# Kernel optimization log

Measured on AMD Instinct MI355X. Metric: run time of the kernel, lower is better.

## Reference

```python
import jax, jax.numpy as jnp
import numpy as np

V, E, H = 50000, 256, 256   # vocab, emb_dim, hid_dim
R, S, W = 64, 32, 64        # reviews, sentences/review, words/sentence
UF = 20                     # user feature dim


def _bigru_last(x, wih, whh, bih, bhh):
    """Bidirectional GRU over x [B,T,D]; returns sum of final hidden states of
    the two directions, shape [B,H]. Params stacked over direction axis 0."""
    Hh = whh.shape[-1]

    def onedir(xd, wi, wh, bi, bh):
        gx = jnp.einsum('btd,gd->btg', xd, wi) + bi  # [B,T,3H] input gates precomputed

        def step(h, gxt):
            gh = h @ wh.T + bh
            r = jax.nn.sigmoid(gxt[:, :Hh] + gh[:, :Hh])
            z = jax.nn.sigmoid(gxt[:, Hh:2 * Hh] + gh[:, Hh:2 * Hh])
            n = jnp.tanh(gxt[:, 2 * Hh:] + r * gh[:, 2 * Hh:])
            return (1.0 - z) * n + z * h, None

        h0 = jnp.zeros((xd.shape[0], Hh), xd.dtype)
        hT, _ = jax.lax.scan(step, h0, jnp.swapaxes(gx, 0, 1))
        return hT

    return (onedir(x, wih[0], whh[0], bih[0], bhh[0])
            + onedir(x[:, ::-1], wih[1], whh[1], bih[1], bhh[1]))


def setup_inputs() -> dict:
    key = jax.random.key(0)
    ks = iter(jax.random.split(key, 40))

    def wmat(shape, scale=0.05):
        return jax.random.normal(next(ks), shape, jnp.float32) * scale

    inp = {}
    inp['inputs'] = jax.random.randint(next(ks), (R, S, W), 0, V)
    inp['sent_lengths'] = jax.random.randint(next(ks), (R, S), 1, W)
    inp['sent_counts'] = jax.random.randint(next(ks), (R,), 1, S)
    inp['user_feats'] = jax.random.normal(next(ks), (R, UF), jnp.float32)
    inp['embed'] = wmat((V, E))
    for name, din in (('wg', E), ('sg', H), ('rg', H + UF)):
        inp[name + '_wih'] = wmat((2, 3 * H, din))
        inp[name + '_whh'] = wmat((2, 3 * H, H))
        inp[name + '_bih'] = jnp.zeros((2, 3 * H), jnp.float32)
        inp[name + '_bhh'] = jnp.zeros((2, 3 * H), jnp.float32)
    inp['rfc_w1'] = wmat((H // 2, H + UF)); inp['rfc_b1'] = jnp.zeros((H // 2,), jnp.float32)
    inp['rfc_w2'] = wmat((1, H // 2));      inp['rfc_b2'] = jnp.zeros((1,), jnp.float32)
    inp['pfc_w1'] = wmat((H // 2, H));      inp['pfc_b1'] = jnp.zeros((H // 2,), jnp.float32)
    inp['pfc_w2'] = wmat((9, H // 2));      inp['pfc_b2'] = jnp.zeros((9,), jnp.float32)
    inp['uf_w'] = jnp.ones((UF,), jnp.float32)  # user_feats_weights
    return inp


def reference(inputs, sent_lengths, sent_counts, user_feats, embed,
              wg_wih, wg_whh, wg_bih, wg_bhh,
              sg_wih, sg_whh, sg_bih, sg_bhh,
              rg_wih, rg_whh, rg_bih, rg_bhh,
              rfc_w1, rfc_b1, rfc_w2, rfc_b2,
              pfc_w1, pfc_b1, pfc_w2, pfc_b2, uf_w):
    Rr, Sr, Wr = inputs.shape
    emb = embed[inputs]  # [R,S,W,E]  (dropout = identity in eval mode)
    # word-level bi-GRU, all R*S sentences batched together
    sent = _bigru_last(emb.reshape(Rr * Sr, Wr, emb.shape[-1]),
                       wg_wih, wg_whh, wg_bih, wg_bhh).reshape(Rr, Sr, -1)
    # sentence-level bi-GRU, batch over reviews
    rev = _bigru_last(sent, sg_wih, sg_whh, sg_bih, sg_bhh)  # [R,H]
    # F.normalize(user_feats) * user_feats_weights
    nrm = jnp.maximum(jnp.linalg.norm(user_feats, axis=-1, keepdims=True), 1e-12)
    p_batch = jnp.concatenate([rev, (user_feats / nrm) * uf_w], axis=-1)  # [R,H+20]
    r_stars = (jax.nn.selu(p_batch @ rfc_w1.T + rfc_b1) @ rfc_w2.T + rfc_b2)[:, 0]  # [R]
    # review-level bi-GRU over the sequence of reviews (batch 1)
    doc = _bigru_last(p_batch[None], rg_wih, rg_whh, rg_bih, rg_bhh)[0]  # [H]
    p_stars = jax.nn.selu(doc @ pfc_w1.T + pfc_b1) @ pfc_w2.T + pfc_b2  # [9]
    return p_stars, r_stars
```

## Files before the change

kernel.cpp:

```cpp
#include <hip/hip_runtime.h>
#include <math.h>

#define R_ 64
#define S_ 32
#define W_ 64
#define H_ 256
#define UF_ 20
#define TC 4

typedef short bf16x8 __attribute__((ext_vector_type(8)));
typedef float f32x4  __attribute__((ext_vector_type(4)));

#define MFMA(a,b,c) __builtin_amdgcn_mfma_f32_16x16x32_bf16((a),(b),(c),0,0,0)

typedef const unsigned int __attribute__((address_space(1)))* gp_t;
typedef unsigned int __attribute__((address_space(3)))* lp_t;
#define GLOAD16(SRC, DST) \
  __builtin_amdgcn_global_load_lds((gp_t)(const void*)(SRC), (lp_t)(void*)(DST), 16, 0, 0)

#define SW(r) ((((r)>>1)&7)<<3)

#define BFRAG(ff) ((ff) < 40 ? Breg[(ff) < 40 ? (ff) : 0] \
                 : *(const bf16x8*)&Bl[w][(ff) >= 40 ? (ff)-40 : 0][l*8])

__device__ __forceinline__ float sigf(float x){ return 1.0f/(1.0f+__expf(-x)); }
__device__ __forceinline__ float tanhf_(float x){ float e=__expf(2.0f*x); return 1.0f-2.0f/(e+1.0f); }
__device__ __forceinline__ float seluf_(float x){
  const float sc=1.0507009873554805f, al=1.6732632423543772f;
  return x>0.0f ? sc*x : sc*al*(expf(x)-1.0f);
}
__device__ __forceinline__ short tobf(float f){
  unsigned u=__float_as_uint(f); u += 0x7fffu + ((u>>16)&1u); return (short)(u>>16);
}
__device__ __forceinline__ float bf2f(short s){
  return __uint_as_float(((unsigned)(unsigned short)s) << 16);
}
__device__ __forceinline__ unsigned pk2(float a, float b){
  return (unsigned)(unsigned short)tobf(a) | ((unsigned)(unsigned short)tobf(b) << 16);
}

__global__ void prep_word_w(const float* __restrict__ wih, const float* __restrict__ whh,
                            short* __restrict__ Bw)
{
  int idx = blockIdx.x*256 + threadIdx.x;
  int lane = idx & 63;
  int rest = idx >> 6;
  int f  = rest % 6;  rest /= 6;
  int kt = rest % 16; rest /= 16;
  int w  = rest % 8;
  int d  = rest / 8;
  int gate = f >> 1;
  int j = 32*w + (f&1)*16 + (lane&15);
  int row = gate*256 + j;
  const float* W = (kt < 8 ? wih : whh) + (size_t)d*768*256;
  int k = (kt&7)*32 + (lane>>4)*8;
  short* dst = Bw + ((((size_t)(d*8 + w)*16 + kt)*6 + f)*64 + lane)*8;
#pragma unroll
  for (int jj=0;jj<8;jj++) dst[jj] = tobf(W[(size_t)row*256 + k + jj]);
}

__global__ void prep_rnn_w(const float* __restrict__ whh, short* __restrict__ Bs)
{
  int idx = blockIdx.x*256 + threadIdx.x;
  int lane = idx & 63;
  int rest = idx >> 6;
  int f  = rest % 6; rest /= 6;
  int kt = rest % 8; rest /= 8;
  int w  = rest % 8;
  int d  = rest / 8;
  int j = 32*w + (f&1)*16 + (lane&15);
  int row = (f>>1)*256 + j;
  const float* W = whh + (size_t)d*768*256;
  int k = kt*32 + (lane>>4)*8;
  short* dst = Bs + ((((size_t)(d*8 + w)*8 + kt)*6 + f)*64 + lane)*8;
#pragma unroll
  for (int jj=0;jj<8;jj++) dst[jj] = tobf(W[(size_t)row*256 + k + jj]);
}

__global__ void prep_gemm_w(const float* __restrict__ Wsrc, short* __restrict__ Bg)
{
  int idx = blockIdx.x*256 + threadIdx.x;
  int lane = idx & 63;
  int rest = idx >> 6;
  int kt = rest % 8;
  int nt = rest / 8;
  int n = nt*16 + (lane&15);
  int k = kt*32 + (lane>>4)*8;
  short* dst = Bg + (((size_t)nt*8 + kt)*64 + lane)*8;
#pragma unroll
  for (int jj=0;jj<8;jj++) dst[jj] = tobf(Wsrc[(size_t)n*256 + k + jj]);
}

__global__ void prep_embb(const float* __restrict__ E, short* __restrict__ O, int M)
{
  const int t = blockIdx.x*256 + threadIdx.x;
  const int row = t >> 5, c0 = (t & 31)*8;
  const int r = row < M ? row : M - 1;
  const float* s = E + (size_t)r*256 + c0;
  float4 v0 = *(const float4*)(s);
  float4 v1 = *(const float4*)(s + 4);
  uint4 u;
  u.x = pk2(v0.x, v0.y); u.y = pk2(v0.z, v0.w);
  u.z = pk2(v1.x, v1.y); u.w = pk2(v1.z, v1.w);
  *(uint4*)&O[(size_t)row*256 + c0] = u;
}

__global__ __launch_bounds__(256) void gemm_gxu(
    const short* __restrict__ Ab, const float* __restrict__ Af,
    const int* __restrict__ toks, const short* __restrict__ Bg,
    const float* __restrict__ bih, const float* __restrict__ bhh,
    short* __restrict__ C, long Czoff,
    int mode, int t0, int Mclamp, int Cstride)
{
  const int z  = blockIdx.z;
  const int m0 = blockIdx.x * 64;
  const int yt = blockIdx.y * 8;
  const int ntb = (mode == 2 ? z*48 : 0) + yt;
  const int tid = threadIdx.x;
  const int w = tid >> 6, l = tid & 63;
  const int c = l & 15, q = l >> 4;
  __shared__ short As[64][264];
  {
    const int row = tid >> 2, c0 = (tid & 3) * 64;
    if (mode == 0) {
      const uint4* s = (const uint4*)(Ab + (size_t)(m0+row)*256 + c0);
#pragma unroll
      for (int i = 0; i < 8; i++) *(uint4*)&As[row][c0 + i*8] = s[i];
    } else {
      int r;
      if (mode == 1) {
        r = m0 + row; if (r >= Mclamp) r = Mclamp - 1;
      } else {
        const int rr = m0 + row;
        const int s_ = rr / TC, i_ = rr % TC;
        const int wd = z ? (63 - (t0 + i_)) : (t0 + i_);
        r = toks[s_*64 + wd];
      }
      const float* s = Af + (size_t)r*256 + c0;
#pragma unroll
      for (int i = 0; i < 8; i++) {
        float4 v0 = *(const float4*)(s + i*8);
        float4 v1 = *(const float4*)(s + i*8 + 4);
        uint4 u;
        u.x = pk2(v0.x, v0.y); u.y = pk2(v0.z, v0.w);
        u.z = pk2(v1.x, v1.y); u.w = pk2(v1.z, v1.w);
        *(uint4*)&As[row][c0 + i*8] = u;
      }
    }
  }
  float bias[2];
#pragma unroll
  for (int nt = 0; nt < 2; nt++) {
    const int coln = (yt + 2*w + nt)*16 + c;
    const int bidx = (mode == 2 ? z*768 : 0) + coln;
    bias[nt] = bih[bidx] + ((bidx % 768) < 512 ? bhh[bidx] : 0.0f);
  }
  __syncthreads();
  f32x4 acc[4][2];
#pragma unroll
  for (int a = 0; a < 4; a++) { acc[a][0] = (f32x4)0.f; acc[a][1] = (f32x4)0.f; }
#pragma unroll
  for (int kt = 0; kt < 8; kt++) {
    const int ko = kt*32 + q*8;
    bf16x8 a0 = *(const bf16x8*)&As[ 0+c][ko];
    bf16x8 a1 = *(const bf16x8*)&As[16+c][ko];
    bf16x8 a2 = *(const bf16x8*)&As[32+c][ko];
    bf16x8 a3 = *(const bf16x8*)&As[48+c][ko];
    bf16x8 b0 = *(const bf16x8*)&Bg[(((size_t)(ntb + 2*w    )*8 + kt)*64 + l)*8];
    bf16x8 b1 = *(const bf16x8*)&Bg[(((size_t)(ntb + 2*w + 1)*8 + kt)*64 + l)*8];
    acc[0][0]=MFMA(a0,b0,acc[0][0]); acc[1][0]=MFMA(a1,b0,acc[1][0]);
    acc[2][0]=MFMA(a2,b0,acc[2][0]); acc[3][0]=MFMA(a3,b0,acc[3][0]);
    acc[0][1]=MFMA(a0,b1,acc[0][1]); acc[1][1]=MFMA(a1,b1,acc[1][1]);
    acc[2][1]=MFMA(a2,b1,acc[2][1]); acc[3][1]=MFMA(a3,b1,acc[3][1]);
  }
  short* Cz = C + (size_t)z * Czoff;
#pragma unroll
  for (int mt = 0; mt < 4; mt++)
#pragma unroll
  for (int nt = 0; nt < 2; nt++)
#pragma unroll
  for (int rg = 0; rg < 4; rg++)
    Cz[(size_t)(m0 + mt*16 + q*4 + rg)*Cstride + (yt + 2*w + nt)*16 + c] =
        tobf(acc[mt][nt][rg] + bias[nt]);
}

__device__ __forceinline__ void stage_issue(
    short* dstbase,
    int mode, int d, int g, int w, int l,
    int nwords, int t0, int tt,
    const int* tokp, const short* gxF, const short* gxB)
{
  const char* bF = (const char*)gxF;
  const char* bB = (const char*)gxB;
#pragma unroll
  for (int i = 0; i < 3; i++) {
    const int off = i*1024 + l*16;
    const int rl  = (off >= 1536) ? 1 : 0;
    const int col = off - rl*1536;
    const char* src;
    if (mode == 0) {
      const int tx  = d ? (nwords - 1 - tt) : tt;
      const int tok = tokp[(2*w + rl)*64 + tx];
      src = bF + (size_t)tok*3072 + d*1536 + col;
    } else if (mode == 1) {
      const int ri = (g*16 + 2*w + rl)*TC + (tt - t0);
      src = (d ? bB : bF) + (size_t)ri*1536 + col;
    } else {
      const int se  = d ? (nwords - 1 - tt) : tt;
      const int row = g*16 + 2*w + rl;
      src = bF + ((size_t)row*nwords + se)*3072 + (size_t)d*1536 + col;
    }
    GLOAD16(src, dstbase + (size_t)w*1536 + i*512);
  }
}

__global__ __launch_bounds__(512, 2) void gru_rec(
    const int* __restrict__ toks,
    const short* __restrict__ gxF, const short* __restrict__ gxB,
    const short* __restrict__ Bh, int wstride, int koff,
    const float* __restrict__ bhh,
    float* __restrict__ hstate, int NS,
    int t0, int nsteps, int mode, int nwords)
{
  const int d = blockIdx.x & 1;
  const int g = blockIdx.x >> 1;
  const int tid = threadIdx.x;
  const int w = tid >> 6, l = tid & 63;
  const int c = l & 15, q = l >> 4;

  __shared__ short gbuf[2][16][768];
  __shared__ short hbf[2][16][264];
  __shared__ short Bl[8][8][512];
  __shared__ int   tokL[1024];

  if (mode == 0)
    for (int i = tid; i < 1024; i += 512) tokL[i] = toks[(size_t)g*1024 + i];

  bf16x8 Breg[40];
  {
    const short* Bb = Bh + (size_t)(d*8 + w)*wstride + (size_t)koff*3072 + l*8;
#pragma unroll
    for (int ff = 0; ff < 48; ff++) {
      bf16x8 v = *(const bf16x8*)(Bb + ff*512);
      if (ff < 40) Breg[ff] = v;
      else *(bf16x8*)&Bl[w][ff-40][l*8] = v;
    }
  }

  float bNH[2];
#pragma unroll
  for (int jt = 0; jt < 2; jt++)
    bNH[jt] = bhh[d*768 + 512 + 32*w + jt*16 + c];

  float hst[2][4];
  const int cur0 = t0 & 1;
  if (t0 == 0) {
#pragma unroll
    for (int a = 0; a < 2; a++)
#pragma unroll
    for (int r = 0; r < 4; r++) hst[a][r] = 0.0f;
  } else {
#pragma unroll
    for (int jt = 0; jt < 2; jt++)
#pragma unroll
    for (int rg = 0; rg < 4; rg++)
      hst[jt][rg] = hstate[((size_t)d*NS + g*16 + q*4 + rg)*256 + 32*w + jt*16 + c];
  }
#pragma unroll
  for (int jt = 0; jt < 2; jt++)
#pragma unroll
  for (int rg = 0; rg < 4; rg++)
    hbf[cur0][q*4 + rg][32*w + jt*16 + c] = tobf(hst[jt][rg]);

  stage_issue((short*)gbuf[cur0], mode, d, g, w, l, nwords, t0, t0,
              (mode == 0) ? toks + (size_t)g*1024 : (const int*)nullptr, gxF, gxB);

  __syncthreads();

  const int tend = t0 + nsteps;
  for (int t = t0; t < tend; t++) {
    const int cur = t & 1, nxt = 1 - cur;

    if (t + 1 < tend)
      stage_issue((short*)gbuf[nxt], mode, d, g, w, l, nwords, t0, t + 1,
                  tokL, gxF, gxB);

    f32x4 accR[2], accZ[2], accNH[2];
#pragma unroll
    for (int a = 0; a < 2; a++) { accR[a]=(f32x4)0.f; accZ[a]=(f32x4)0.f; accNH[a]=(f32x4)0.f; }
#pragma unroll
    for (int kt = 0; kt < 8; kt++) {
      bf16x8 a0 = *(const bf16x8*)&hbf[cur][c][kt*32 + q*8];
      bf16x8 b0 = BFRAG(kt*6+0), b1 = BFRAG(kt*6+1), b2 = BFRAG(kt*6+2),
             b3 = BFRAG(kt*6+3), b4 = BFRAG(kt*6+4), b5 = BFRAG(kt*6+5);
      accR[0]=MFMA(a0,b0,accR[0]);  accR[1]=MFMA(a0,b1,accR[1]);
      accZ[0]=MFMA(a0,b2,accZ[0]);  accZ[1]=MFMA(a0,b3,accZ[1]);
      accNH[0]=MFMA(a0,b4,accNH[0]); accNH[1]=MFMA(a0,b5,accNH[1]);
    }

#pragma unroll
    for (int jt = 0; jt < 2; jt++)
#pragma unroll
    for (int rg = 0; rg < 4; rg++) {
      const int m = q*4 + rg;
      const int j = 32*w + jt*16 + c;
      const float gr = bf2f(gbuf[cur][m][j]);
      const float gz = bf2f(gbuf[cur][m][256 + j]);
      const float gn = bf2f(gbuf[cur][m][512 + j]);
      const float r = sigf(gr + accR[jt][rg]);
      const float z = sigf(gz + accZ[jt][rg]);
      const float n = tanhf_(gn + r*(accNH[jt][rg] + bNH[jt]));
      float h = hst[jt][rg];
      h = (1.0f - z)*n + z*h;
      hst[jt][rg] = h;
      hbf[nxt][m][j] = tobf(h);
    }
    __syncthreads();
  }

#pragma unroll
  for (int jt = 0; jt < 2; jt++)
#pragma unroll
  for (int rg = 0; rg < 4; rg++)
    hstate[((size_t)d*NS + g*16 + q*4 + rg)*256 + 32*w + jt*16 + c] = hst[jt][rg];
}

__global__ void add2bf(const float* __restrict__ a, const float* __restrict__ b,
                       short* __restrict__ o)
{
  int i = (blockIdx.x*256 + threadIdx.x)*4;
  float4 x = *(const float4*)&a[i];
  float4 y = *(const float4*)&b[i];
  *(uint2*)&o[i] = make_uint2(pk2(x.x+y.x, x.y+y.y), pk2(x.z+y.z, x.w+y.w));
}

__global__ __launch_bounds__(512, 2) void rev_gru(
    const float* __restrict__ gx, const short* __restrict__ Br,
    const float* __restrict__ bhh,
    float* __restrict__ doc)
{
  const int d = blockIdx.x;
  const int tid = threadIdx.x;
  const int w = tid >> 6, l = tid & 63;
  const int c = l & 15, q = l >> 4;
  const int j0 = 32*w + c;

  __shared__ short hbf[2][16][256];
  __shared__ short Bl[8][8][512];
  for (int i = tid; i < 2*16*256; i += 512) ((short*)hbf)[i] = 0;

  bf16x8 Breg[40];
  {
    const short* Bbase = Br + (size_t)(d*8 + w)*8*6*512 + l*8;
#pragma unroll
    for (int ff = 0; ff < 48; ff++) {
      bf16x8 v = *(const bf16x8*)(Bbase + ff*512);
      if (ff < 40) Breg[ff] = v;
      else *(bf16x8*)&Bl[w][ff-40][l*8] = v;
    }
  }

  float bNH[2];
#pragma unroll
  for (int jt = 0; jt < 2; jt++)
    bNH[jt] = bhh[d*768 + 512 + j0 + jt*16];

  float hst[2];
  hst[0] = 0.0f; hst[1] = 0.0f;
  __syncthreads();

  for (int t = 0; t < 64; t++) {
    const int cur = t & 1, nxt = 1 - cur;
    const int teff = (d == 0) ? t : (63 - t);

    float G[2][3];
    if (q == 0) {
#pragma unroll
      for (int jt = 0; jt < 2; jt++) {
        const size_t row = (size_t)teff*1536 + d*768;
        const int j = j0 + jt*16;
        G[jt][0] = gx[row + j]; G[jt][1] = gx[row + 256 + j]; G[jt][2] = gx[row + 512 + j];
      }
    }

    f32x4 accR[2], accZ[2], accNH[2];
#pragma unroll
    for (int a=0;a<2;a++) { accR[a]=(f32x4)0.f; accZ[a]=(f32x4)0.f; accNH[a]=(f32x4)0.f; }
#pragma unroll
    for (int kt = 0; kt < 8; kt++) {
      bf16x8 a0 = *(const bf16x8*)&hbf[cur][c][(kt*32 + q*8) ^ SW(c)];
      bf16x8 b0 = BFRAG(kt*6+0), b1 = BFRAG(kt*6+1), b2 = BFRAG(kt*6+2),
             b3 = BFRAG(kt*6+3), b4 = BFRAG(kt*6+4), b5 = BFRAG(kt*6+5);
      accR[0]=MFMA(a0,b0,accR[0]);  accR[1]=MFMA(a0,b1,accR[1]);
      accZ[0]=MFMA(a0,b2,accZ[0]);  accZ[1]=MFMA(a0,b3,accZ[1]);
      accNH[0]=MFMA(a0,b4,accNH[0]); accNH[1]=MFMA(a0,b5,accNH[1]);
    }

    if (q == 0) {
#pragma unroll
      for (int jt = 0; jt < 2; jt++) {
        const float r = sigf(G[jt][0] + accR[jt][0]);
        const float z = sigf(G[jt][1] + accZ[jt][0]);
        const float n = tanhf_(G[jt][2] + r*(accNH[jt][0] + bNH[jt]));
        const float h = n + z*(hst[jt] - n);
        hst[jt] = h;
        hbf[nxt][0][j0 + jt*16] = tobf(h);
      }
    }
    __syncthreads();
  }
  if (q == 0) {
#pragma unroll
    for (int jt = 0; jt < 2; jt++)
      doc[d*256 + j0 + jt*16] = hst[jt];
  }
}

__global__ __launch_bounds__(256) void gemm_nt16(
    const float* __restrict__ A, const float* __restrict__ B,
    const float* __restrict__ bih, const float* __restrict__ bhh,
    float* __restrict__ C, int M, int N, int K)
{
  const int m0 = blockIdx.x * 16;
  const int n0 = blockIdx.y * 64;
  const int tid = threadIdx.x;
  __shared__ float As[16][17];
  __shared__ float Bs[16][68];
  float acc[4] = {0,0,0,0};
  const int m  = tid >> 4, n4 = (tid & 15) * 4;
  const int bn = tid >> 2, bk = (tid & 3) * 4;
  for (int k0 = 0; k0 < K; k0 += 16) {
    const int ak = tid & 15;
    float av = (k0 + ak < K) ? A[(size_t)(m0+m)*K + k0 + ak] : 0.0f;
    float4 b4 = make_float4(0,0,0,0);
    if (k0 + bk < K) b4 = *(const float4*)&B[(size_t)(n0+bn)*K + k0 + bk];
    __syncthreads();
    As[ak][m] = av;
    Bs[bk+0][bn]=b4.x; Bs[bk+1][bn]=b4.y; Bs[bk+2][bn]=b4.z; Bs[bk+3][bn]=b4.w;
    __syncthreads();
#pragma unroll
    for (int k = 0; k < 16; k++) {
      const float a = As[k][m];
      const float4 bb = *(const float4*)&Bs[k][n4];
      acc[0]+=a*bb.x; acc[1]+=a*bb.y; acc[2]+=a*bb.z; acc[3]+=a*bb.w;
    }
  }
#pragma unroll
  for (int i = 0; i < 4; i++) {
    const int n = n0 + n4 + i;
    acc[i] += bih[n] + ((n % 768) < 512 ? bhh[n] : 0.0f);
  }
  *(float4*)&C[(size_t)(m0+m)*N + n0+n4] = make_float4(acc[0],acc[1],acc[2],acc[3]);
}

__global__ void pbrs_k(const float* __restrict__ hs, const float* __restrict__ uf,
                       const float* __restrict__ ufw,
                       const float* __restrict__ w1, const float* __restrict__ b1,
                       const float* __restrict__ w2, const float* __restrict__ b2,
                       float* __restrict__ pb, float* __restrict__ out)
{
  const int r = blockIdx.x, tid = threadIdx.x;
  __shared__ float ps[276];
  __shared__ float s1[128];
  __shared__ float nrm;
  if (tid == 0) {
    float s = 0.f;
    for (int i = 0; i < UF_; i++) { const float v = uf[r*UF_ + i]; s += v*v; }
    nrm = fmaxf(sqrtf(s), 1e-12f);
  }
  __syncthreads();
  if (tid < H_) {
    const float v = hs[r*H_ + tid] + hs[(size_t)R_*H_ + r*H_ + tid];
    ps[tid] = v; pb[r*276 + tid] = v;
  }
  if (tid < UF_) {
    const float v = uf[r*UF_ + tid] / nrm * ufw[tid];
    ps[H_ + tid] = v; pb[r*276 + H_ + tid] = v;
  }
  __syncthreads();
  if (tid < 128) {
    float a = b1[tid];
    for (int k = 0; k < 276; k++) a += ps[k] * w1[tid*276 + k];
    s1[tid] = seluf_(a);
  }
  __syncthreads();
  if (tid == 0) {
    float s = b2[0];
    for (int k = 0; k < 128; k++) s += s1[k] * w2[k];
    out[9 + r] = s;
  }
}

__global__ void pstars_k(const float* __restrict__ doc2,
                         const float* __restrict__ w1, const float* __restrict__ b1,
                         const float* __restrict__ w2, const float* __restrict__ b2,
                         float* __restrict__ out)
{
  const int tid = threadIdx.x;
  __shared__ float dc[256];
  __shared__ float s1[128];
  dc[tid]       = doc2[tid]       + doc2[256 + tid];
  dc[128 + tid] = doc2[128 + tid] + doc2[384 + tid];
  __syncthreads();
  float a = b1[tid];
  for (int k = 0; k < 256; k++) a += dc[k] * w1[tid*256 + k];
  s1[tid] = seluf_(a);
  __syncthreads();
  if (tid < 9) {
    float s = b2[tid];
    for (int k = 0; k < 128; k++) s += s1[k] * w2[tid*128 + k];
    out[tid] = s;
  }
}

extern "C" void kernel_launch(void* const* d_in, const int* in_sizes, int n_in,
                              void* d_out, int out_size, void* d_ws, size_t ws_size,
                              hipStream_t stream)
{
  const int*   toks   = (const int*)  d_in[0];
  const float* uf     = (const float*)d_in[3];
  const float* embed  = (const float*)d_in[4];
  const float* wg_wih = (const float*)d_in[5];
  const float* wg_whh = (const float*)d_in[6];
  const float* wg_bih = (const float*)d_in[7];
  const float* wg_bhh = (const float*)d_in[8];
  const float* sg_wih = (const float*)d_in[9];
  const float* sg_whh = (const float*)d_in[10];
  const float* sg_bih = (const float*)d_in[11];
  const float* sg_bhh = (const float*)d_in[12];
  const float* rg_wih = (const float*)d_in[13];
  const float* rg_whh = (const float*)d_in[14];
  const float* rg_bih = (const float*)d_in[15];
  const float* rg_bhh = (const float*)d_in[16];
  const float* rfc_w1 = (const float*)d_in[17];
  const float* rfc_b1 = (const float*)d_in[18];
  const float* rfc_w2 = (const float*)d_in[19];
  const float* rfc_b2 = (const float*)d_in[20];
  const float* pfc_w1 = (const float*)d_in[21];
  const float* pfc_b1 = (const float*)d_in[22];
  const float* pfc_w2 = (const float*)d_in[23];
  const float* pfc_b2 = (const float*)d_in[24];
  const float* uf_w   = (const float*)d_in[25];
  float* out = (float*)d_out;
  float* ws  = (float*)d_ws;
  (void)in_sizes; (void)n_in; (void)out_size;

  const size_t OFF_BW   = 0;
  const size_t OFF_BS   = OFF_BW  + 393216;
  const size_t OFF_BR   = OFF_BS  + 196608;
  const size_t OFF_BG   = OFF_BR  + 196608;
  const size_t OFF_BGW  = OFF_BG  + 196608;
  const size_t OFF_HF   = OFF_BGW + 196608;
  const size_t OFF_SB   = OFF_HF  + 1048576;
  const size_t OFF_GXS  = OFF_SB  + 262144;
  const size_t OFF_HS   = OFF_GXS + 1572864;
  const size_t OFF_PB   = OFF_HS  + 32768;
  const size_t OFF_GXR  = OFF_PB  + 17664;
  const size_t OFF_DOC  = OFF_GXR + 98304;
  const size_t OFF_GXT  = OFF_DOC + 512;
  const size_t TOT_A    = OFF_GXT + (size_t)50048*1536/2;
  const size_t OFF_EMB  = TOT_A;
  const size_t TOT_B    = TOT_A + (size_t)50048*256/2;

  short* Bw   = (short*)(ws + OFF_BW);
  short* Bs   = (short*)(ws + OFF_BS);
  short* Br   = (short*)(ws + OFF_BR);
  short* Bg   = (short*)(ws + OFF_BG);
  short* Bgw  = (short*)(ws + OFF_BGW);
  float* hfin = ws + OFF_HF;
  short* sentb= (short*)(ws + OFF_SB);
  short* gxs  = (short*)(ws + OFF_GXS);
  float* hs   = ws + OFF_HS;
  float* pb   = ws + OFF_PB;
  float* gxr  = ws + OFF_GXR;
  float* doc  = ws + OFF_DOC;
  short* gxf  = (short*)(ws + OFF_GXT);
  short* gxb  = gxf + (size_t)8192*768;
  short* gxv  = (short*)(ws + OFF_GXT);
  short* embb = (short*)(ws + OFF_EMB);

  const bool bigger = ws_size >= TOT_B * sizeof(float);
  const bool big    = ws_size >= TOT_A * sizeof(float);

  prep_word_w<<<384, 256, 0, stream>>>(wg_wih, wg_whh, Bw);
  prep_rnn_w<<<192, 256, 0, stream>>>(sg_whh, Bs);
  prep_rnn_w<<<192, 256, 0, stream>>>(rg_whh, Br);
  prep_gemm_w<<<192, 256, 0, stream>>>(sg_wih, Bg);
  prep_gemm_w<<<192, 256, 0, stream>>>(wg_wih, Bgw);

  if (big) {
    if (bigger) {
      prep_embb<<<6256, 256, 0, stream>>>(embed, embb, 50000);
      gemm_gxu<<<dim3(782, 12, 1), 256, 0, stream>>>(
          embb, nullptr, nullptr, Bgw, wg_bih, wg_bhh, gxv, 0, 0, 0, 0, 1536);
    } else {
      gemm_gxu<<<dim3(782, 12, 1), 256, 0, stream>>>(
          nullptr, embed, nullptr, Bgw, wg_bih, wg_bhh, gxv, 0, 1, 0, 50000, 1536);
    }
    gru_rec<<<256, 512, 0, stream>>>(toks, gxv, nullptr, Bw, 49152, 8,
        wg_bhh, hfin, 2048, 0, 64, 0, 64);
  } else {
    for (int tc = 0; tc < 64/TC; tc++) {
      gemm_gxu<<<dim3(128, 6, 2), 256, 0, stream>>>(
          nullptr, embed, toks, Bgw, wg_bih, wg_bhh, gxf, (long)8192*768, 2, tc*TC, 0, 768);
      gru_rec<<<256, 512, 0, stream>>>(toks, gxf, gxb, Bw, 49152, 8,
          wg_bhh, hfin, 2048, tc*TC, TC, 1, 64);
    }
  }
  add2bf<<<512, 256, 0, stream>>>(hfin, hfin + (size_t)2048*256, sentb);

  gemm_gxu<<<dim3(32, 12, 1), 256, 0, stream>>>(
      sentb, nullptr, nullptr, Bg, sg_bih, sg_bhh, gxs, 0, 0, 0, 2048, 1536);
  gru_rec<<<8, 512, 0, stream>>>(nullptr, gxs, nullptr, Bs, 24576, 0,
      sg_bhh, hs, 64, 0, 32, 2, 32);

  pbrs_k<<<R_, 256, 0, stream>>>(hs, uf, uf_w, rfc_w1, rfc_b1, rfc_w2, rfc_b2, pb, out);

  gemm_nt16<<<dim3(4, 24), 256, 0, stream>>>(pb, rg_wih, rg_bih, rg_bhh, gxr, 64, 1536, 276);
  rev_gru<<<2, 512, 0, stream>>>(gxr, Br, rg_bhh, doc);
  pstars_k<<<1, 128, 0, stream>>>(doc, pfc_w1, pfc_b1, pfc_w2, pfc_b2, out);
}
```

Measured before the change: 669.1 us.

## Merge prep kernels, fuse add2bf and review input GEMM, swap grid order

Folds the five weight-prep kernels and the embedding conversion into one launch, folds the add-of-directions bf16 conversion into the sentence GEMM's A-tile load (new mode 3), and computes the review-GRU input projection inside pbrs_k instead of a separate GEMM. It also swaps the grid of the big vocabulary GEMM so the N tiles vary fastest, which may improve reuse of the A rows. The aim is to cut launch overhead and intermediate buffer traffic. In exchange pbrs_k now runs 1536 serial 276-long dot products across only 64 blocks, which could be slower than the old tiled GEMM.

After: 713.1 us. +6.6%, slower.

```diff
diff --git a/kernel.cpp b/kernel.cpp
--- a/kernel.cpp
+++ b/kernel.cpp
@@ -39,10 +39,9 @@
   return (unsigned)(unsigned short)tobf(a) | ((unsigned)(unsigned short)tobf(b) << 16);
 }
 
-__global__ void prep_word_w(const float* __restrict__ wih, const float* __restrict__ whh,
-                            short* __restrict__ Bw)
-{
-  int idx = blockIdx.x*256 + threadIdx.x;
+__device__ __forceinline__ void prep_word_body(int idx, const float* wih,
+                                               const float* whh, short* Bw)
+{
   int lane = idx & 63;
   int rest = idx >> 6;
   int f  = rest % 6;  rest /= 6;
@@ -59,9 +58,8 @@
   for (int jj=0;jj<8;jj++) dst[jj] = tobf(W[(size_t)row*256 + k + jj]);
 }
 
-__global__ void prep_rnn_w(const float* __restrict__ whh, short* __restrict__ Bs)
-{
-  int idx = blockIdx.x*256 + threadIdx.x;
+__device__ __forceinline__ void prep_rnn_body(int idx, const float* whh, short* Bs)
+{
   int lane = idx & 63;
   int rest = idx >> 6;
   int f  = rest % 6; rest /= 6;
@@ -77,9 +75,8 @@
   for (int jj=0;jj<8;jj++) dst[jj] = tobf(W[(size_t)row*256 + k + jj]);
 }
 
-__global__ void prep_gemm_w(const float* __restrict__ Wsrc, short* __restrict__ Bg)
-{
-  int idx = blockIdx.x*256 + threadIdx.x;
+__device__ __forceinline__ void prep_gemm_body(int idx, const float* Wsrc, short* Bg)
+{
   int lane = idx & 63;
   int rest = idx >> 6;
   int kt = rest % 8;
@@ -91,9 +88,8 @@
   for (int jj=0;jj<8;jj++) dst[jj] = tobf(Wsrc[(size_t)n*256 + k + jj]);
 }
 
-__global__ void prep_embb(const float* __restrict__ E, short* __restrict__ O, int M)
-{
-  const int t = blockIdx.x*256 + threadIdx.x;
+__device__ __forceinline__ void prep_embb_body(int t, const float* E, short* O, int M)
+{
   const int row = t >> 5, c0 = (t & 31)*8;
   const int r = row < M ? row : M - 1;
   const float* s = E + (size_t)r*256 + c0;
@@ -105,16 +101,34 @@
   *(uint4*)&O[(size_t)row*256 + c0] = u;
 }
 
+__global__ void prep_all(const float* __restrict__ wg_wih, const float* __restrict__ wg_whh,
+                         const float* __restrict__ sg_whh, const float* __restrict__ rg_whh,
+                         const float* __restrict__ sg_wih, const float* __restrict__ embed,
+                         short* __restrict__ Bw, short* __restrict__ Bs,
+                         short* __restrict__ Br, short* __restrict__ Bg,
+                         short* __restrict__ Bgw, short* __restrict__ embb)
+{
+  const int b = blockIdx.x, tid = threadIdx.x;
+  if      (b <  384) prep_word_body( b       *256 + tid, wg_wih, wg_whh, Bw);
+  else if (b <  576) prep_rnn_body ((b- 384)*256 + tid, sg_whh, Bs);
+  else if (b <  768) prep_rnn_body ((b- 576)*256 + tid, rg_whh, Br);
+  else if (b <  960) prep_gemm_body((b- 768)*256 + tid, sg_wih, Bg);
+  else if (b < 1152) prep_gemm_body((b- 960)*256 + tid, wg_wih, Bgw);
+  else               prep_embb_body((b-1152)*256 + tid, embed, embb, 50000);
+}
+
 __global__ __launch_bounds__(256) void gemm_gxu(
     const short* __restrict__ Ab, const float* __restrict__ Af,
     const int* __restrict__ toks, const short* __restrict__ Bg,
     const float* __restrict__ bih, const float* __restrict__ bhh,
     short* __restrict__ C, long Czoff,
-    int mode, int t0, int Mclamp, int Cstride)
+    int mode, int t0, int Mclamp, int Cstride, int swapxy)
 {
   const int z  = blockIdx.z;
-  const int m0 = blockIdx.x * 64;
-  const int yt = blockIdx.y * 8;
+  const int bx = swapxy ? blockIdx.y : blockIdx.x;
+  const int by = swapxy ? blockIdx.x : blockIdx.y;
+  const int m0 = bx * 64;
+  const int yt = by * 8;
   const int ntb = (mode == 2 ? z*48 : 0) + yt;
   const int tid = threadIdx.x;
   const int w = tid >> 6, l = tid & 63;
@@ -126,6 +140,20 @@
       const uint4* s = (const uint4*)(Ab + (size_t)(m0+row)*256 + c0);
 #pragma unroll
       for (int i = 0; i < 8; i++) *(uint4*)&As[row][c0 + i*8] = s[i];
+    } else if (mode == 3) {
+      const float* s0 = Af + (size_t)(m0+row)*256 + c0;
+      const float* s1 = s0 + (size_t)2048*256;
+#pragma unroll
+      for (int i = 0; i < 8; i++) {
+        float4 a0 = *(const float4*)(s0 + i*8);
+        float4 a1 = *(const float4*)(s0 + i*8 + 4);
+        float4 b0 = *(const float4*)(s1 + i*8);
+        float4 b1 = *(const float4*)(s1 + i*8 + 4);
+        uint4 u;
+        u.x = pk2(a0.x+b0.x, a0.y+b0.y); u.y = pk2(a0.z+b0.z, a0.w+b0.w);
+        u.z = pk2(a1.x+b1.x, a1.y+b1.y); u.w = pk2(a1.z+b1.z, a1.w+b1.w);
+        *(uint4*)&As[row][c0 + i*8] = u;
+      }
     } else {
       int r;
       if (mode == 1) {
@@ -325,15 +353,6 @@
     hstate[((size_t)d*NS + g*16 + q*4 + rg)*256 + 32*w + jt*16 + c] = hst[jt][rg];
 }
 
-__global__ void add2bf(const float* __restrict__ a, const float* __restrict__ b,
-                       short* __restrict__ o)
-{
-  int i = (blockIdx.x*256 + threadIdx.x)*4;
-  float4 x = *(const float4*)&a[i];
-  float4 y = *(const float4*)&b[i];
-  *(uint2*)&o[i] = make_uint2(pk2(x.x+y.x, x.y+y.y), pk2(x.z+y.z, x.w+y.w));
-}
-
 __global__ __launch_bounds__(512, 2) void rev_gru(
     const float* __restrict__ gx, const short* __restrict__ Br,
     const float* __restrict__ bhh,
@@ -416,48 +435,13 @@
   }
 }
 
-__global__ __launch_bounds__(256) void gemm_nt16(
-    const float* __restrict__ A, const float* __restrict__ B,
-    const float* __restrict__ bih, const float* __restrict__ bhh,
-    float* __restrict__ C, int M, int N, int K)
-{
-  const int m0 = blockIdx.x * 16;
-  const int n0 = blockIdx.y * 64;
-  const int tid = threadIdx.x;
-  __shared__ float As[16][17];
-  __shared__ float Bs[16][68];
-  float acc[4] = {0,0,0,0};
-  const int m  = tid >> 4, n4 = (tid & 15) * 4;
-  const int bn = tid >> 2, bk = (tid & 3) * 4;
-  for (int k0 = 0; k0 < K; k0 += 16) {
-    const int ak = tid & 15;
-    float av = (k0 + ak < K) ? A[(size_t)(m0+m)*K + k0 + ak] : 0.0f;
-    float4 b4 = make_float4(0,0,0,0);
-    if (k0 + bk < K) b4 = *(const float4*)&B[(size_t)(n0+bn)*K + k0 + bk];
-    __syncthreads();
-    As[ak][m] = av;
-    Bs[bk+0][bn]=b4.x; Bs[bk+1][bn]=b4.y; Bs[bk+2][bn]=b4.z; Bs[bk+3][bn]=b4.w;
-    __syncthreads();
-#pragma unroll
-    for (int k = 0; k < 16; k++) {
-      const float a = As[k][m];
-      const float4 bb = *(const float4*)&Bs[k][n4];
-      acc[0]+=a*bb.x; acc[1]+=a*bb.y; acc[2]+=a*bb.z; acc[3]+=a*bb.w;
-    }
-  }
-#pragma unroll
-  for (int i = 0; i < 4; i++) {
-    const int n = n0 + n4 + i;
-    acc[i] += bih[n] + ((n % 768) < 512 ? bhh[n] : 0.0f);
-  }
-  *(float4*)&C[(size_t)(m0+m)*N + n0+n4] = make_float4(acc[0],acc[1],acc[2],acc[3]);
-}
-
 __global__ void pbrs_k(const float* __restrict__ hs, const float* __restrict__ uf,
                        const float* __restrict__ ufw,
                        const float* __restrict__ w1, const float* __restrict__ b1,
                        const float* __restrict__ w2, const float* __restrict__ b2,
-                       float* __restrict__ pb, float* __restrict__ out)
+                       const float* __restrict__ rgw, const float* __restrict__ rgbih,
+                       const float* __restrict__ rgbhh,
+                       float* __restrict__ gxr, float* __restrict__ out)
 {
   const int r = blockIdx.x, tid = threadIdx.x;
   __shared__ float ps[276];
@@ -469,15 +453,19 @@
     nrm = fmaxf(sqrtf(s), 1e-12f);
   }
   __syncthreads();
-  if (tid < H_) {
-    const float v = hs[r*H_ + tid] + hs[(size_t)R_*H_ + r*H_ + tid];
-    ps[tid] = v; pb[r*276 + tid] = v;
-  }
-  if (tid < UF_) {
-    const float v = uf[r*UF_ + tid] / nrm * ufw[tid];
-    ps[H_ + tid] = v; pb[r*276 + H_ + tid] = v;
-  }
-  __syncthreads();
+  if (tid < H_)
+    ps[tid] = hs[r*H_ + tid] + hs[(size_t)R_*H_ + r*H_ + tid];
+  if (tid < UF_)
+    ps[H_ + tid] = uf[r*UF_ + tid] / nrm * ufw[tid];
+  __syncthreads();
+#pragma unroll
+  for (int i = 0; i < 6; i++) {
+    const int n = tid + 256*i;
+    float a = rgbih[n] + ((n % 768) < 512 ? rgbhh[n] : 0.0f);
+    const float* wr = rgw + (size_t)n*276;
+    for (int k = 0; k < 276; k++) a += ps[k] * wr[k];
+    gxr[(size_t)r*1536 + n] = a;
+  }
   if (tid < 128) {
     float a = b1[tid];
     for (int k = 0; k < 276; k++) a += ps[k] * w1[tid*276 + k];
@@ -568,10 +556,8 @@
   short* Bg   = (short*)(ws + OFF_BG);
   short* Bgw  = (short*)(ws + OFF_BGW);
   float* hfin = ws + OFF_HF;
-  short* sentb= (short*)(ws + OFF_SB);
   short* gxs  = (short*)(ws + OFF_GXS);
   float* hs   = ws + OFF_HS;
-  float* pb   = ws + OFF_PB;
   float* gxr  = ws + OFF_GXR;
   float* doc  = ws + OFF_DOC;
   short* gxf  = (short*)(ws + OFF_GXT);
@@ -582,41 +568,37 @@
   const bool bigger = ws_size >= TOT_B * sizeof(float);
   const bool big    = ws_size >= TOT_A * sizeof(float);
 
-  prep_word_w<<<384, 256, 0, stream>>>(wg_wih, wg_whh, Bw);
-  prep_rnn_w<<<192, 256, 0, stream>>>(sg_whh, Bs);
-  prep_rnn_w<<<192, 256, 0, stream>>>(rg_whh, Br);
-  prep_gemm_w<<<192, 256, 0, stream>>>(sg_wih, Bg);
-  prep_gemm_w<<<192, 256, 0, stream>>>(wg_wih, Bgw);
+  prep_all<<<1152 + (bigger ? 6256 : 0), 256, 0, stream>>>(
+      wg_wih, wg_whh, sg_whh, rg_whh, sg_wih, embed,
+      Bw, Bs, Br, Bg, Bgw, embb);
 
   if (big) {
     if (bigger) {
-      prep_embb<<<6256, 256, 0, stream>>>(embed, embb, 50000);
-      gemm_gxu<<<dim3(782, 12, 1), 256, 0, stream>>>(
-          embb, nullptr, nullptr, Bgw, wg_bih, wg_bhh, gxv, 0, 0, 0, 0, 1536);
+      gemm_gxu<<<dim3(12, 782, 1), 256, 0, stream>>>(
+          embb, nullptr, nullptr, Bgw, wg_bih, wg_bhh, gxv, 0, 0, 0, 0, 1536, 1);
     } else {
-      gemm_gxu<<<dim3(782, 12, 1), 256, 0, stream>>>(
-          nullptr, embed, nullptr, Bgw, wg_bih, wg_bhh, gxv, 0, 1, 0, 50000, 1536);
+      gemm_gxu<<<dim3(12, 782, 1), 256, 0, stream>>>(
+          nullptr, embed, nullptr, Bgw, wg_bih, wg_bhh, gxv, 0, 1, 0, 50000, 1536, 1);
     }
     gru_rec<<<256, 512, 0, stream>>>(toks, gxv, nullptr, Bw, 49152, 8,
         wg_bhh, hfin, 2048, 0, 64, 0, 64);
   } else {
     for (int tc = 0; tc < 64/TC; tc++) {
       gemm_gxu<<<dim3(128, 6, 2), 256, 0, stream>>>(
-          nullptr, embed, toks, Bgw, wg_bih, wg_bhh, gxf, (long)8192*768, 2, tc*TC, 0, 768);
+          nullptr, embed, toks, Bgw, wg_bih, wg_bhh, gxf, (long)8192*768, 2, tc*TC, 0, 768, 0);
       gru_rec<<<256, 512, 0, stream>>>(toks, gxf, gxb, Bw, 49152, 8,
           wg_bhh, hfin, 2048, tc*TC, TC, 1, 64);
     }
   }
-  add2bf<<<512, 256, 0, stream>>>(hfin, hfin + (size_t)2048*256, sentb);
 
   gemm_gxu<<<dim3(32, 12, 1), 256, 0, stream>>>(
-      sentb, nullptr, nullptr, Bg, sg_bih, sg_bhh, gxs, 0, 0, 0, 2048, 1536);
+      nullptr, hfin, nullptr, Bg, sg_bih, sg_bhh, gxs, 0, 3, 0, 0, 1536, 0);
   gru_rec<<<8, 512, 0, stream>>>(nullptr, gxs, nullptr, Bs, 24576, 0,
       sg_bhh, hs, 64, 0, 32, 2, 32);
 
-  pbrs_k<<<R_, 256, 0, stream>>>(hs, uf, uf_w, rfc_w1, rfc_b1, rfc_w2, rfc_b2, pb, out);
-
-  gemm_nt16<<<dim3(4, 24), 256, 0, stream>>>(pb, rg_wih, rg_bih, rg_bhh, gxr, 64, 1536, 276);
+  pbrs_k<<<R_, 256, 0, stream>>>(hs, uf, uf_w, rfc_w1, rfc_b1, rfc_w2, rfc_b2,
+                                 rg_wih, rg_bih, rg_bhh, gxr, out);
+
   rev_gru<<<2, 512, 0, stream>>>(gxr, Br, rg_bhh, doc);
   pstars_k<<<1, 128, 0, stream>>>(doc, pfc_w1, pfc_b1, pfc_w2, pfc_b2, out);
 }
```
